# Performance work log

Hardware: AMD Instinct MI355X
Metric: run time of the kernel (lower is better)

Reference implementation:

```python
import jax, jax.numpy as jnp
import numpy as np

B, C, F_IN, F_OUT = 2048, 63, 250, 250
NEG_SLOPE = 0.2
N = B * C  # flattened node count


def _build_edge_index():
    # fixed fully-connected (no self) graph over the FIRST 63 nodes only
    src = np.array([i for i in range(C) for j in range(C) if i != j], dtype=np.int32)
    dst = np.array([j for i in range(C) for j in range(C) if i != j], dtype=np.int32)
    # PyG GATConv add_self_loops=True: self loop for every node (num_nodes = N)
    loops = np.arange(N, dtype=np.int32)
    src = np.concatenate([src, loops])
    dst = np.concatenate([dst, loops])
    return jnp.asarray(np.stack([src, dst]))  # [2, E]


def setup_inputs() -> dict:
    key = jax.random.key(0)
    kx, kw, ks, kd = jax.random.split(key, 4)
    x = jax.random.normal(kx, (B, 1, C, F_IN), dtype=jnp.float32)
    # GATConv params (heads=1): lin weight, att_src, att_dst, bias
    W = jax.random.normal(kw, (F_IN, F_OUT), dtype=jnp.float32) / np.sqrt(F_IN)
    att_src = jax.random.normal(ks, (F_OUT,), dtype=jnp.float32) / np.sqrt(F_OUT)
    att_dst = jax.random.normal(kd, (F_OUT,), dtype=jnp.float32) / np.sqrt(F_OUT)
    bias = jnp.zeros((F_OUT,), dtype=jnp.float32)
    return {"x": x, "W": W, "att_src": att_src, "att_dst": att_dst,
            "bias": bias, "edge_index": _build_edge_index()}


def reference(x, W, att_src, att_dst, bias, edge_index):
    b, _, c, f = x.shape
    n = b * c
    h = x.reshape(n, f) @ W                      # [N, F_OUT]
    a_src = h @ att_src                          # [N]
    a_dst = h @ att_dst                          # [N]
    src, dst = edge_index[0], edge_index[1]
    e = jax.nn.leaky_relu(a_src[src] + a_dst[dst], NEG_SLOPE)  # [E]
    # segment softmax over incoming edges of each dst node (stable)
    m = jax.ops.segment_max(e, dst, num_segments=n)
    ex = jnp.exp(e - m[dst])
    denom = jax.ops.segment_sum(ex, dst, num_segments=n)
    alpha = ex / denom[dst]                      # [E]
    out = jax.ops.segment_sum(alpha[:, None] * h[src], dst, num_segments=n)
    out = out + bias
    return out.reshape(b, 1, c, -1)              # [B,1,63,F_OUT]
```

## Files before the change

kernel.cpp:

```cpp
#include <hip/hip_runtime.h>
#include <cstdint>
#include <cstddef>

#define M_TOTAL 129024
#define KDIM    250
#define NDIM    250
#define BM      32
#define TPB     4
#define NBLK    1008
#define TILE_F  (BM*KDIM)

typedef float  f32x4  __attribute__((ext_vector_type(4)));
typedef float  f32x2  __attribute__((ext_vector_type(2)));
typedef __bf16 bf16x8 __attribute__((ext_vector_type(8)));

static __device__ __forceinline__ unsigned short f2bf(float f) {
  unsigned u = __float_as_uint(f);
  u += 0x7fffu + ((u >> 16) & 1u);
  return (unsigned short)(u >> 16);
}

static __device__ __forceinline__ float wsum(float v) {
#pragma unroll
  for (int o = 32; o > 0; o >>= 1) v += __shfl_xor(v, o, 64);
  return v;
}
static __device__ __forceinline__ float wmaxr(float v) {
#pragma unroll
  for (int o = 32; o > 0; o >>= 1) v = fmaxf(v, __shfl_xor(v, o, 64));
  return v;
}

static __device__ __forceinline__ void gll16(const float* g, float* l) {
  __builtin_amdgcn_global_load_lds(
      (const __attribute__((address_space(1))) void*)g,
      (__attribute__((address_space(3))) void*)l, 16, 0, 0);
}
static __device__ __forceinline__ void gll4(const float* g, float* l) {
  __builtin_amdgcn_global_load_lds(
      (const __attribute__((address_space(1))) void*)g,
      (__attribute__((address_space(3))) void*)l, 4, 0, 0);
}

__global__ void wcvt_kernel(const float* __restrict__ W, unsigned short* __restrict__ WTf) {
  const int f     = blockIdx.x * 256 + threadIdx.x;
  const int lane  = f & 63;
  const int kk    = (f >> 6) & 7;
  const int ntile = f >> 9;
  const int n     = ntile * 16 + (lane & 15);
  const int k0    = kk * 32 + (lane >> 4) * 8;
  unsigned u[4];
#pragma unroll
  for (int p = 0; p < 4; ++p) {
    const int ka = k0 + 2 * p, kb = k0 + 2 * p + 1;
    unsigned short a = (n < NDIM && ka < KDIM) ? f2bf(W[(size_t)ka * NDIM + n]) : 0;
    unsigned short b = (n < NDIM && kb < KDIM) ? f2bf(W[(size_t)kb * NDIM + n]) : 0;
    u[p] = (unsigned)a | ((unsigned)b << 16);
  }
  *reinterpret_cast<uint4*>(WTf + (size_t)f * 8) = make_uint4(u[0], u[1], u[2], u[3]);
}

__global__ __launch_bounds__(256, 2) void gemm_kernel(
    const float* __restrict__ X, const unsigned short* __restrict__ WTf,
    const float* __restrict__ bias, float* __restrict__ out,
    float* __restrict__ h63) {
  __shared__ __attribute__((aligned(16))) float lX[TILE_F + 8];
  __shared__ __attribute__((aligned(16))) float lO[TILE_F];

  const int tid  = threadIdx.x;
  const int lane = tid & 63;
  const int w    = tid >> 6;
  const int r16  = lane & 15;
  const int quad = lane >> 4;

  if (tid < 8) lX[TILE_F + tid] = 0.f;

  bf16x8 wf[4][8];
#pragma unroll
  for (int ft = 0; ft < 4; ++ft)
#pragma unroll
    for (int kk = 0; kk < 8; ++kk)
      wf[ft][kk] = *reinterpret_cast<const bf16x8*>(
          WTf + (size_t)((((w * 4 + ft) * 8) + kk) * 64 + lane) * 8);

  float bv[4][4];
#pragma unroll
  for (int ft = 0; ft < 4; ++ft)
#pragma unroll
    for (int i = 0; i < 4; ++i) {
      const int c = w * 64 + ft * 16 + quad * 4 + i;
      bv[ft][i] = (c < NDIM) ? bias[c] : 0.f;
    }

  const int tile0 = blockIdx.x * TPB;

  auto stage = [&](int g) {
    const float* gb = X + (size_t)g * TILE_F;
    if (w < 3) {
#pragma unroll
      for (int c = 0; c < 8; ++c) {
        const int ch = w * 8 + c;
        gll16(gb + ch * 256 + lane * 4, lX + ch * 256);
      }
    } else {
#pragma unroll
      for (int c = 0; c < 7; ++c) {
        const int ch = 24 + c;
        gll16(gb + ch * 256 + lane * 4, lX + ch * 256);
      }
      gll4(gb + 7936 + lane, lX + 7936);
    }
  };

  stage(tile0);

  for (int t = 0; t < TPB; ++t) {
    __syncthreads();

    f32x4 acc[4][2];
#pragma unroll
    for (int ft = 0; ft < 4; ++ft)
#pragma unroll
      for (int nt = 0; nt < 2; ++nt) acc[ft][nt] = f32x4{0.f, 0.f, 0.f, 0.f};

#pragma unroll
    for (int kk = 0; kk < 8; ++kk) {
      bf16x8 xf[2];
#pragma unroll
      for (int nt = 0; nt < 2; ++nt) {
        const float* p = lX + (size_t)(nt * 16 + r16) * KDIM + kk * 32 + quad * 8;
        const f32x2 a = *reinterpret_cast<const f32x2*>(p);
        const f32x2 b = *reinterpret_cast<const f32x2*>(p + 2);
        const f32x2 c = *reinterpret_cast<const f32x2*>(p + 4);
        const f32x2 d = *reinterpret_cast<const f32x2*>(p + 6);
        bf16x8 v;
        v[0] = (__bf16)a.x; v[1] = (__bf16)a.y;
        v[2] = (__bf16)b.x; v[3] = (__bf16)b.y;
        v[4] = (__bf16)c.x; v[5] = (__bf16)c.y;
        v[6] = (__bf16)d.x; v[7] = (__bf16)d.y;
        xf[nt] = v;
      }
#pragma unroll
      for (int ft = 0; ft < 4; ++ft)
#pragma unroll
        for (int nt = 0; nt < 2; ++nt)
          acc[ft][nt] = __builtin_amdgcn_mfma_f32_16x16x32_bf16(
              wf[ft][kk], xf[nt], acc[ft][nt], 0, 0, 0);
    }

    const int rbase = (tile0 + t) * BM;
#pragma unroll
    for (int ft = 0; ft < 4; ++ft) {
      const int c0 = w * 64 + ft * 16 + quad * 4;
#pragma unroll
      for (int nt = 0; nt < 2; ++nt) {
        const int row = nt * 16 + r16;
        float* o = lO + (size_t)row * KDIM + c0;
        const f32x4 a = acc[ft][nt];
        if (c0 + 3 < NDIM) {
          *reinterpret_cast<f32x2*>(o)     = f32x2{a.x + bv[ft][0], a.y + bv[ft][1]};
          *reinterpret_cast<f32x2*>(o + 2) = f32x2{a.z + bv[ft][2], a.w + bv[ft][3]};
        } else if (c0 + 1 < NDIM) {
          *reinterpret_cast<f32x2*>(o) = f32x2{a.x + bv[ft][0], a.y + bv[ft][1]};
        }
      }
    }
    if (rbase < 63) {
#pragma unroll
      for (int ft = 0; ft < 4; ++ft) {
        const int c0 = w * 64 + ft * 16 + quad * 4;
#pragma unroll
        for (int nt = 0; nt < 2; ++nt) {
          const int row = rbase + nt * 16 + r16;
          if (row < 63) {
            const f32x4 a = acc[ft][nt];
#pragma unroll
            for (int i = 0; i < 4; ++i)
              if (c0 + i < NDIM) h63[(size_t)row * NDIM + c0 + i] = a[i];
          }
        }
      }
    }

    __syncthreads();
    if (t + 1 < TPB) stage(tile0 + t + 1);

    float* ob = out + (size_t)(tile0 + t) * TILE_F;
#pragma unroll
    for (int c = 0; c < 8; ++c) {
      const int flat = c * 1024 + tid * 4;
      if (c < 7 || tid < 208) {
        const f32x4 v = *reinterpret_cast<const f32x4*>(lO + flat);
        __builtin_nontemporal_store(v, reinterpret_cast<f32x4*>(ob + flat));
      }
    }
  }
}

__global__ void att_kernel(const float* __restrict__ h, const float* __restrict__ att_src,
                           const float* __restrict__ att_dst, const float* __restrict__ bias,
                           float* __restrict__ out) {
  const int d = blockIdx.x;
  const int tid = threadIdx.x;
  const int lane = tid & 63;
  const int wid = tid >> 6;

  __shared__ float s_asrc[64];
  __shared__ float s_adst;
  __shared__ float s_alpha[64];

  for (int s = wid; s < 63; s += 4) {
    float sum = 0.f;
    for (int f = lane; f < NDIM; f += 64) sum += h[s * NDIM + f] * att_src[f];
    sum = wsum(sum);
    if (lane == 0) s_asrc[s] = sum;
  }
  if (wid == 0) {
    float sum = 0.f;
    for (int f = lane; f < NDIM; f += 64) sum += h[d * NDIM + f] * att_dst[f];
    sum = wsum(sum);
    if (lane == 0) s_adst = sum;
  }
  __syncthreads();

  if (wid == 0) {
    float e = -__builtin_inff();
    if (lane < 63) {
      float x = s_asrc[lane] + s_adst;
      e = (x > 0.f) ? x : 0.2f * x;
    }
    const float m = wmaxr(e);
    const float p = (lane < 63) ? expf(e - m) : 0.f;
    const float den = wsum(p);
    s_alpha[lane] = p / den;
  }
  __syncthreads();

  const int f = tid;
  if (f < NDIM) {
    float o = bias[f];
    for (int s = 0; s < 63; ++s) o += s_alpha[s] * h[s * NDIM + f];
    out[(size_t)d * NDIM + f] = o;
  }
}

extern "C" void kernel_launch(void* const* d_in, const int* in_sizes, int n_in,
                              void* d_out, int out_size, void* d_ws, size_t ws_size,
                              hipStream_t stream) {
  const float* X       = (const float*)d_in[0];
  const float* W       = (const float*)d_in[1];
  const float* att_src = (const float*)d_in[2];
  const float* att_dst = (const float*)d_in[3];
  const float* bias    = (const float*)d_in[4];
  float* out = (float*)d_out;

  unsigned short* WTf = (unsigned short*)d_ws;
  float* h63 = (float*)((char*)d_ws + 131072);

  wcvt_kernel<<<32, 256, 0, stream>>>(W, WTf);
  gemm_kernel<<<NBLK, 256, 0, stream>>>(X, WTf, bias, out, h63);
  att_kernel<<<63, 256, 0, stream>>>(h63, att_src, att_dst, bias, out);
}
```

Before: 274.1 us.

## Use one tile per block, stream weights per k-step, store output directly

Each block now handles a single 32-row tile instead of four, which removes the staged prefetch loop and raises the launch-bounds occupancy target to 4 blocks per CU. Weight fragments are no longer held in registers for the whole block. They are loaded from global memory with a one-step-ahead double buffer inside a non-unrolled k loop. The LDS output staging buffer is gone, and results are written straight to global memory with 8-byte nontemporal stores. This cuts LDS and register pressure to allow more resident blocks, at the cost of repeated weight reads per block, less coalesced output writes, and no overlap of the next tile's load with compute.

```diff
diff --git a/kernel.cpp b/kernel.cpp
--- a/kernel.cpp
+++ b/kernel.cpp
@@ -6,8 +6,7 @@
 #define KDIM    250
 #define NDIM    250
 #define BM      32
-#define TPB     4
-#define NBLK    1008
+#define NBLK    4032
 #define TILE_F  (BM*KDIM)
 
 typedef float  f32x4  __attribute__((ext_vector_type(4)));
@@ -60,12 +59,11 @@
   *reinterpret_cast<uint4*>(WTf + (size_t)f * 8) = make_uint4(u[0], u[1], u[2], u[3]);
 }
 
-__global__ __launch_bounds__(256, 2) void gemm_kernel(
+__global__ __launch_bounds__(256, 4) void gemm_kernel(
     const float* __restrict__ X, const unsigned short* __restrict__ WTf,
     const float* __restrict__ bias, float* __restrict__ out,
     float* __restrict__ h63) {
   __shared__ __attribute__((aligned(16))) float lX[TILE_F + 8];
-  __shared__ __attribute__((aligned(16))) float lO[TILE_F];
 
   const int tid  = threadIdx.x;
   const int lane = tid & 63;
@@ -75,13 +73,23 @@
 
   if (tid < 8) lX[TILE_F + tid] = 0.f;
 
-  bf16x8 wf[4][8];
-#pragma unroll
-  for (int ft = 0; ft < 4; ++ft)
-#pragma unroll
-    for (int kk = 0; kk < 8; ++kk)
-      wf[ft][kk] = *reinterpret_cast<const bf16x8*>(
-          WTf + (size_t)((((w * 4 + ft) * 8) + kk) * 64 + lane) * 8);
+  {
+    const float* gb = X + (size_t)blockIdx.x * TILE_F;
+    if (w < 3) {
+#pragma unroll
+      for (int c = 0; c < 8; ++c) {
+        const int ch = w * 8 + c;
+        gll16(gb + ch * 256 + lane * 4, lX + ch * 256);
+      }
+    } else {
+#pragma unroll
+      for (int c = 0; c < 7; ++c) {
+        const int ch = 24 + c;
+        gll16(gb + ch * 256 + lane * 4, lX + ch * 256);
+      }
+      gll4(gb + 7936 + lane, lX + 7936);
+    }
+  }
 
   float bv[4][4];
 #pragma unroll
@@ -92,106 +100,88 @@
       bv[ft][i] = (c < NDIM) ? bias[c] : 0.f;
     }
 
-  const int tile0 = blockIdx.x * TPB;
-
-  auto stage = [&](int g) {
-    const float* gb = X + (size_t)g * TILE_F;
-    if (w < 3) {
-#pragma unroll
-      for (int c = 0; c < 8; ++c) {
-        const int ch = w * 8 + c;
-        gll16(gb + ch * 256 + lane * 4, lX + ch * 256);
-      }
-    } else {
-#pragma unroll
-      for (int c = 0; c < 7; ++c) {
-        const int ch = 24 + c;
-        gll16(gb + ch * 256 + lane * 4, lX + ch * 256);
-      }
-      gll4(gb + 7936 + lane, lX + 7936);
-    }
-  };
-
-  stage(tile0);
-
-  for (int t = 0; t < TPB; ++t) {
-    __syncthreads();
-
-    f32x4 acc[4][2];
+  __syncthreads();
+
+  f32x4 acc[4][2];
+#pragma unroll
+  for (int ft = 0; ft < 4; ++ft)
+#pragma unroll
+    for (int nt = 0; nt < 2; ++nt) acc[ft][nt] = f32x4{0.f, 0.f, 0.f, 0.f};
+
+  const unsigned short* wp = WTf + (size_t)(((w * 4) * 8) * 64 + lane) * 8;
+  const size_t ft_str = (size_t)8 * 64 * 8;
+  const size_t kk_str = (size_t)64 * 8;
+
+  bf16x8 wc[4], wn[4];
+#pragma unroll
+  for (int ft = 0; ft < 4; ++ft)
+    wc[ft] = *reinterpret_cast<const bf16x8*>(wp + ft * ft_str);
+
+#pragma unroll 1
+  for (int kk = 0; kk < 8; ++kk) {
+    if (kk < 7) {
+#pragma unroll
+      for (int ft = 0; ft < 4; ++ft)
+        wn[ft] = *reinterpret_cast<const bf16x8*>(wp + ft * ft_str + (kk + 1) * kk_str);
+    }
+    bf16x8 xf[2];
+#pragma unroll
+    for (int nt = 0; nt < 2; ++nt) {
+      const float* p = lX + (size_t)(nt * 16 + r16) * KDIM + kk * 32 + quad * 8;
+      const f32x2 a = *reinterpret_cast<const f32x2*>(p);
+      const f32x2 b = *reinterpret_cast<const f32x2*>(p + 2);
+      const f32x2 c = *reinterpret_cast<const f32x2*>(p + 4);
+      const f32x2 d = *reinterpret_cast<const f32x2*>(p + 6);
+      bf16x8 v;
+      v[0] = (__bf16)a.x; v[1] = (__bf16)a.y;
+      v[2] = (__bf16)b.x; v[3] = (__bf16)b.y;
+      v[4] = (__bf16)c.x; v[5] = (__bf16)c.y;
+      v[6] = (__bf16)d.x; v[7] = (__bf16)d.y;
+      xf[nt] = v;
+    }
 #pragma unroll
     for (int ft = 0; ft < 4; ++ft)
 #pragma unroll
-      for (int nt = 0; nt < 2; ++nt) acc[ft][nt] = f32x4{0.f, 0.f, 0.f, 0.f};
-
-#pragma unroll
-    for (int kk = 0; kk < 8; ++kk) {
-      bf16x8 xf[2];
-#pragma unroll
-      for (int nt = 0; nt < 2; ++nt) {
-        const float* p = lX + (size_t)(nt * 16 + r16) * KDIM + kk * 32 + quad * 8;
-        const f32x2 a = *reinterpret_cast<const f32x2*>(p);
-        const f32x2 b = *reinterpret_cast<const f32x2*>(p + 2);
-        const f32x2 c = *reinterpret_cast<const f32x2*>(p + 4);
-        const f32x2 d = *reinterpret_cast<const f32x2*>(p + 6);
-        bf16x8 v;
-        v[0] = (__bf16)a.x; v[1] = (__bf16)a.y;
-        v[2] = (__bf16)b.x; v[3] = (__bf16)b.y;
-        v[4] = (__bf16)c.x; v[5] = (__bf16)c.y;
-        v[6] = (__bf16)d.x; v[7] = (__bf16)d.y;
-        xf[nt] = v;
-      }
-#pragma unroll
-      for (int ft = 0; ft < 4; ++ft)
-#pragma unroll
-        for (int nt = 0; nt < 2; ++nt)
-          acc[ft][nt] = __builtin_amdgcn_mfma_f32_16x16x32_bf16(
-              wf[ft][kk], xf[nt], acc[ft][nt], 0, 0, 0);
-    }
-
-    const int rbase = (tile0 + t) * BM;
+      for (int nt = 0; nt < 2; ++nt)
+        acc[ft][nt] = __builtin_amdgcn_mfma_f32_16x16x32_bf16(
+            wc[ft], xf[nt], acc[ft][nt], 0, 0, 0);
+#pragma unroll
+    for (int ft = 0; ft < 4; ++ft) wc[ft] = wn[ft];
+  }
+
+  const int rbase = blockIdx.x * BM;
+#pragma unroll
+  for (int ft = 0; ft < 4; ++ft) {
+    const int c0 = w * 64 + ft * 16 + quad * 4;
+#pragma unroll
+    for (int nt = 0; nt < 2; ++nt) {
+      const int row = rbase + nt * 16 + r16;
+      float* o = out + (size_t)row * NDIM + c0;
+      const f32x4 a = acc[ft][nt];
+      if (c0 + 3 < NDIM) {
+        __builtin_nontemporal_store(f32x2{a.x + bv[ft][0], a.y + bv[ft][1]},
+                                    reinterpret_cast<f32x2*>(o));
+        __builtin_nontemporal_store(f32x2{a.z + bv[ft][2], a.w + bv[ft][3]},
+                                    reinterpret_cast<f32x2*>(o + 2));
+      } else if (c0 + 1 < NDIM) {
+        __builtin_nontemporal_store(f32x2{a.x + bv[ft][0], a.y + bv[ft][1]},
+                                    reinterpret_cast<f32x2*>(o));
+      }
+    }
+  }
+  if (blockIdx.x < 2) {
 #pragma unroll
     for (int ft = 0; ft < 4; ++ft) {
       const int c0 = w * 64 + ft * 16 + quad * 4;
 #pragma unroll
       for (int nt = 0; nt < 2; ++nt) {
-        const int row = nt * 16 + r16;
-        float* o = lO + (size_t)row * KDIM + c0;
-        const f32x4 a = acc[ft][nt];
-        if (c0 + 3 < NDIM) {
-          *reinterpret_cast<f32x2*>(o)     = f32x2{a.x + bv[ft][0], a.y + bv[ft][1]};
-          *reinterpret_cast<f32x2*>(o + 2) = f32x2{a.z + bv[ft][2], a.w + bv[ft][3]};
-        } else if (c0 + 1 < NDIM) {
-          *reinterpret_cast<f32x2*>(o) = f32x2{a.x + bv[ft][0], a.y + bv[ft][1]};
+        const int row = rbase + nt * 16 + r16;
+        if (row < 63) {
+          const f32x4 a = acc[ft][nt];
+#pragma unroll
+          for (int i = 0; i < 4; ++i)
+            if (c0 + i < NDIM) h63[(size_t)row * NDIM + c0 + i] = a[i];
         }
-      }
-    }
-    if (rbase < 63) {
-#pragma unroll
-      for (int ft = 0; ft < 4; ++ft) {
-        const int c0 = w * 64 + ft * 16 + quad * 4;
-#pragma unroll
-        for (int nt = 0; nt < 2; ++nt) {
-          const int row = rbase + nt * 16 + r16;
-          if (row < 63) {
-            const f32x4 a = acc[ft][nt];
-#pragma unroll
-            for (int i = 0; i < 4; ++i)
-              if (c0 + i < NDIM) h63[(size_t)row * NDIM + c0 + i] = a[i];
-          }
-        }
-      }
-    }
-
-    __syncthreads();
-    if (t + 1 < TPB) stage(tile0 + t + 1);
-
-    float* ob = out + (size_t)(tile0 + t) * TILE_F;
-#pragma unroll
-    for (int c = 0; c < 8; ++c) {
-      const int flat = c * 1024 + tid * 4;
-      if (c < 7 || tid < 208) {
-        const f32x4 v = *reinterpret_cast<const f32x4*>(lO + flat);
-        __builtin_nontemporal_store(v, reinterpret_cast<f32x4*>(ob + flat));
       }
     }
   }
```

New measurement: 341.4 us. +24.6%, slower.
